# Kernel tuning notes

Hardware: AMD Instinct MI355X
Metric: run time of the kernel (lower is better)

Reference implementation:

```python
import jax, jax.numpy as jnp
import numpy as np

N_NODES = 50000

def _gat_layer(x, src, dst, W, a_l, a_r, bias, alpha, agg, act, n_nodes):
    # x: [N, in]; W: [in, H*F]; a_l, a_r: [H, F]; bias: [H*F]
    H, F = a_l.shape
    z = (x @ W).reshape(n_nodes, H, F)                      # [N,H,F]
    el = jnp.einsum('nhf,hf->nh', z, a_l)                   # [N,H]
    er = jnp.einsum('nhf,hf->nh', z, a_r)                   # [N,H]
    e = jax.nn.leaky_relu(el[src] + er[dst], alpha)         # [E,H]
    # segment softmax over in-edges of each destination node
    m = jax.ops.segment_max(e, dst, num_segments=n_nodes)   # [N,H]
    ex = jnp.exp(e - m[dst])                                # [E,H]
    s = jax.ops.segment_sum(ex, dst, num_segments=n_nodes)  # [N,H]
    attn = ex / jnp.maximum(s[dst], 1e-9)                   # [E,H]
    msg = attn[:, :, None] * z[src]                         # [E,H,F]
    h = jax.ops.segment_sum(msg, dst, num_segments=n_nodes) # [N,H,F]
    # identity residual (in_feats == H*F) as in DGL GATConv
    h = h + x.reshape(n_nodes, -1, F)
    h = h + bias.reshape(1, H, F)
    if agg == 'flatten':
        h = h.reshape(n_nodes, H * F)
    else:  # mean over heads
        h = h.mean(axis=1)
    if act is not None:
        h = act(h)
    return h


def setup_inputs() -> dict:
    key = jax.random.key(0)
    ks = jax.random.split(key, 14)
    N, E, D = N_NODES, 800000, 128
    H, F = 4, 32
    sc_in = 1.0 / np.sqrt(D)
    sc_h = 1.0 / np.sqrt(H * F)
    inp = {
        'feats': jax.random.normal(ks[0], (N, D), jnp.float32),
        'src': jax.random.randint(ks[1], (E,), 0, N),
        'dst': jax.random.randint(ks[2], (E,), 0, N),
        'W1': jax.random.normal(ks[3], (D, H * F), jnp.float32) * sc_in,
        'al1': jax.random.normal(ks[4], (H, F), jnp.float32) * sc_h,
        'ar1': jax.random.normal(ks[5], (H, F), jnp.float32) * sc_h,
        'b1': jnp.zeros((H * F,), jnp.float32),
        'W2': jax.random.normal(ks[6], (H * F, H * F), jnp.float32) * sc_h,
        'al2': jax.random.normal(ks[7], (H, F), jnp.float32) * sc_h,
        'ar2': jax.random.normal(ks[8], (H, F), jnp.float32) * sc_h,
        'b2': jnp.zeros((H * F,), jnp.float32),
        'Wp': jax.random.normal(ks[9], (F, 1), jnp.float32) / np.sqrt(F),
        'bp': jnp.zeros((1,), jnp.float32),
    }
    return inp


def reference(feats, src, dst, W1, al1, ar1, b1, W2, al2, ar2, b2, Wp, bp):
    h = _gat_layer(feats, src, dst, W1, al1, ar1, b1, 0.2, 'flatten', jax.nn.elu, N_NODES)
    h = _gat_layer(h, src, dst, W2, al2, ar2, b2, 0.2, 'mean', None, N_NODES)
    return h @ Wp + bp  # [N, 1]
```

## Files before the change

### kernel.cpp

```cpp
#include <hip/hip_runtime.h>
#include <hip/hip_bf16.h>

#define NN 50000
#define NE 800000
#define HF 128
#define MAXDEG 64

#define OFF_FLAG   0u
#define OFF_Z      16668672u
#define OFF_H1     29468672u
#define OFF_EL     42268672u
#define OFF_ER     43068672u
#define OFF_FILL   54000128u
#define OFF_ADJ2   60000000u

typedef __hip_bfloat16 bf16;
typedef unsigned short us16;

#define SCAT_B 3125
#define GEMM_B 782

typedef __attribute__((ext_vector_type(8))) short bf16x8;
typedef __attribute__((ext_vector_type(4))) float f32x4;

__device__ __forceinline__ float us2f(us16 u) {
  union { unsigned int i; float f; } c; c.i = ((unsigned int)u) << 16; return c.f;
}
__device__ __forceinline__ us16 f2us(float f) {
  bf16 h = __float2bfloat16(f);
  union { bf16 h; us16 u; } c; c.h = h; return c.u;
}
__device__ __forceinline__ float blo(unsigned v) {
  union { unsigned i; float f; } c; c.i = v << 16; return c.f;
}
__device__ __forceinline__ float bhi(unsigned v) {
  union { unsigned i; float f; } c; c.i = v & 0xffff0000u; return c.f;
}
__device__ __forceinline__ unsigned pk2(float a, float b) {
  return (unsigned)f2us(a) | ((unsigned)f2us(b) << 16);
}

__device__ __forceinline__ int detect_f32(const us16* __restrict__ u) {
  int t = threadIdx.x;
  int mx = 0;
  for (int i = t; i < 2048; i += 256) {
    int e = (u[i] >> 7) & 0xFF;
    mx = mx > e ? mx : e;
  }
#pragma unroll
  for (int m = 32; m >= 1; m >>= 1) {
    int o = __shfl_xor(mx, m);
    mx = mx > o ? mx : o;
  }
  __shared__ int sred[4];
  if ((t & 63) == 0) sred[t >> 6] = mx;
  __syncthreads();
  int a = sred[0] > sred[1] ? sred[0] : sred[1];
  int b = sred[2] > sred[3] ? sred[2] : sred[3];
  int r = a > b ? a : b;
  return r >= 135;
}

template <int LAYER>
__global__ __launch_bounds__(256) void k_gemm(
    const void* __restrict__ Xv, const void* __restrict__ Wv,
    const void* __restrict__ alr, const void* __restrict__ arr,
    us16* __restrict__ Z, float* __restrict__ el, float* __restrict__ er,
    const int* __restrict__ src, const int* __restrict__ dst,
    int* __restrict__ fill, int* __restrict__ adj2, int* __restrict__ flagp) {
  if (LAYER == 1) {
    if ((int)blockIdx.x < SCAT_B) {
      int e = blockIdx.x * 256 + threadIdx.x;
      int d = dst[e];
      int r = atomicAdd(&fill[d], 1);
      if (r < MAXDEG) adj2[(d << 6) + r] = src[e];
      return;
    }
  }
  int bx = (LAYER == 1) ? (int)blockIdx.x - SCAT_B : (int)blockIdx.x;

  __shared__ us16 Wl[HF * HF];
  int f;
  if (LAYER == 1) {
    f = detect_f32((const us16*)Wv);
    if (bx == 0 && threadIdx.x == 0) *flagp = f;
  } else {
    f = *flagp;
  }

  int tid = threadIdx.x;
  {
    const float* Wf = (const float*)Wv;
    const us16* Wb = (const us16*)Wv;
    for (int e = tid; e < HF * HF; e += 256) {
      int k = e >> 7, n = e & 127;
      int d = ((((k >> 5) * 8 + (n >> 4)) * 4 + ((k >> 3) & 3)) * 16 + (n & 15)) * 8 + (k & 7);
      Wl[d] = f ? f2us(Wf[e]) : Wb[e];
    }
  }
  __syncthreads();

  int w = tid >> 6;
  int lane = tid & 63;
  int q = lane >> 4;
  int c = lane & 15;
  int m0 = bx * 64 + w * 16;

  int rA = m0 + c;
  if (rA >= NN) rA = NN - 1;
  const us16* xb = (const us16*)Xv + (size_t)rA * HF;
  const float* xf = (const float*)Xv + (size_t)rA * HF;

  f32x4 acc[8] = {};
#pragma unroll
  for (int s = 0; s < 4; ++s) {
    bf16x8 a;
    if (LAYER == 1 && f) {
      float4 v0 = *(const float4*)&xf[s * 32 + q * 8];
      float4 v1 = *(const float4*)&xf[s * 32 + q * 8 + 4];
      union { us16 u[8]; bf16x8 v; } cv;
      cv.u[0] = f2us(v0.x); cv.u[1] = f2us(v0.y);
      cv.u[2] = f2us(v0.z); cv.u[3] = f2us(v0.w);
      cv.u[4] = f2us(v1.x); cv.u[5] = f2us(v1.y);
      cv.u[6] = f2us(v1.z); cv.u[7] = f2us(v1.w);
      a = cv.v;
    } else {
      a = *(const bf16x8*)&xb[s * 32 + q * 8];
    }
#pragma unroll
    for (int t = 0; t < 8; ++t) {
      bf16x8 bb = *(const bf16x8*)&Wl[((((s * 8) + t) * 4 + q) * 16 + c) * 8];
      acc[t] = __builtin_amdgcn_mfma_f32_16x16x32_bf16(a, bb, acc[t], 0, 0, 0);
    }
  }

#pragma unroll
  for (int reg = 0; reg < 4; ++reg) {
    int row = m0 + q * 4 + reg;
    if (row < NN) {
      us16* zrow = Z + (size_t)row * HF;
#pragma unroll
      for (int t = 0; t < 8; ++t) zrow[t * 16 + c] = f2us(acc[t][reg]);
    }
  }

  float alv[8], arv[8];
  {
    const float* alf = (const float*)alr; const us16* alb = (const us16*)alr;
    const float* arf = (const float*)arr; const us16* arb = (const us16*)arr;
#pragma unroll
    for (int t = 0; t < 8; ++t) {
      alv[t] = f ? alf[t * 16 + c] : us2f(alb[t * 16 + c]);
      arv[t] = f ? arf[t * 16 + c] : us2f(arb[t * 16 + c]);
    }
  }
#pragma unroll
  for (int reg = 0; reg < 4; ++reg) {
    int row = m0 + q * 4 + reg;
    float pl[4], pr[4];
#pragma unroll
    for (int h = 0; h < 4; ++h) {
      pl[h] = acc[2 * h][reg] * alv[2 * h] + acc[2 * h + 1][reg] * alv[2 * h + 1];
      pr[h] = acc[2 * h][reg] * arv[2 * h] + acc[2 * h + 1][reg] * arv[2 * h + 1];
    }
#pragma unroll
    for (int m = 1; m < 16; m <<= 1) {
#pragma unroll
      for (int h = 0; h < 4; ++h) {
        pl[h] += __shfl_xor(pl[h], m);
        pr[h] += __shfl_xor(pr[h], m);
      }
    }
    if (row < NN) {
      int cc = c & 3;
      float vl = cc == 0 ? pl[0] : cc == 1 ? pl[1] : cc == 2 ? pl[2] : pl[3];
      float vr = cc == 0 ? pr[0] : cc == 1 ? pr[1] : cc == 2 ? pr[2] : pr[3];
      if (c < 4) el[row * 4 + cc] = vl;
      else if (c < 8) er[row * 4 + cc] = vr;
    }
  }
}

template <int LAYER>
__global__ __launch_bounds__(256) void k_agg(
    const us16* __restrict__ Z, const float* __restrict__ el,
    const float* __restrict__ er, const int* __restrict__ fill,
    const int* __restrict__ adj2, const void* __restrict__ resid,
    const void* __restrict__ bias, us16* __restrict__ Hout,
    const void* __restrict__ Wp, const void* __restrict__ bp,
    void* __restrict__ out, const int* __restrict__ flag) {
  int f = *flag;
  int n = blockIdx.x * 4 + (threadIdx.x >> 6);
  int lane = threadIdx.x & 63;
  int g = lane >> 4;
  int p = lane & 15;
  int hl = p >> 2;
  int f0 = p * 8;
  int deg = fill[n];
  if (deg > MAXDEG) deg = MAXDEG;
  int begin = n << 6;
  float erh = er[n * 4 + hl];

  float acc[8] = {};
  float ssum = 0.f;
  int i = g;
  for (; i + 4 < deg; i += 8) {
    int s0 = adj2[begin + i];
    int s1 = adj2[begin + i + 4];
    float l0 = el[s0 * 4 + hl];
    float l1 = el[s1 * 4 + hl];
    uint4 za = *(const uint4*)&Z[(size_t)s0 * HF + f0];
    uint4 zb = *(const uint4*)&Z[(size_t)s1 * HF + f0];
    float sc0 = l0 + erh; sc0 = sc0 > 0.f ? sc0 : 0.2f * sc0;
    float sc1 = l1 + erh; sc1 = sc1 > 0.f ? sc1 : 0.2f * sc1;
    float ex0 = __expf(sc0);
    float ex1 = __expf(sc1);
    ssum += ex0 + ex1;
    acc[0] = fmaf(ex0, blo(za.x), acc[0]); acc[1] = fmaf(ex0, bhi(za.x), acc[1]);
    acc[2] = fmaf(ex0, blo(za.y), acc[2]); acc[3] = fmaf(ex0, bhi(za.y), acc[3]);
    acc[4] = fmaf(ex0, blo(za.z), acc[4]); acc[5] = fmaf(ex0, bhi(za.z), acc[5]);
    acc[6] = fmaf(ex0, blo(za.w), acc[6]); acc[7] = fmaf(ex0, bhi(za.w), acc[7]);
    acc[0] = fmaf(ex1, blo(zb.x), acc[0]); acc[1] = fmaf(ex1, bhi(zb.x), acc[1]);
    acc[2] = fmaf(ex1, blo(zb.y), acc[2]); acc[3] = fmaf(ex1, bhi(zb.y), acc[3]);
    acc[4] = fmaf(ex1, blo(zb.z), acc[4]); acc[5] = fmaf(ex1, bhi(zb.z), acc[5]);
    acc[6] = fmaf(ex1, blo(zb.w), acc[6]); acc[7] = fmaf(ex1, bhi(zb.w), acc[7]);
  }
  if (i < deg) {
    int s = adj2[begin + i];
    float sc = el[s * 4 + hl] + erh;
    sc = sc > 0.f ? sc : 0.2f * sc;
    float ex = __expf(sc);
    ssum += ex;
    uint4 zq = *(const uint4*)&Z[(size_t)s * HF + f0];
    acc[0] = fmaf(ex, blo(zq.x), acc[0]); acc[1] = fmaf(ex, bhi(zq.x), acc[1]);
    acc[2] = fmaf(ex, blo(zq.y), acc[2]); acc[3] = fmaf(ex, bhi(zq.y), acc[3]);
    acc[4] = fmaf(ex, blo(zq.z), acc[4]); acc[5] = fmaf(ex, bhi(zq.z), acc[5]);
    acc[6] = fmaf(ex, blo(zq.w), acc[6]); acc[7] = fmaf(ex, bhi(zq.w), acc[7]);
  }
  ssum += __shfl_xor(ssum, 16); ssum += __shfl_xor(ssum, 32);
#pragma unroll
  for (int j = 0; j < 8; ++j) {
    acc[j] += __shfl_xor(acc[j], 16);
    acc[j] += __shfl_xor(acc[j], 32);
  }
  float inv = 1.f / fmaxf(ssum, 1e-9f);

  float rx[8];
  if (LAYER == 1 && f) {
    const float* rf = (const float*)resid + (size_t)n * HF + f0;
    float4 r0 = *(const float4*)rf;
    float4 r1 = *(const float4*)(rf + 4);
    rx[0] = r0.x; rx[1] = r0.y; rx[2] = r0.z; rx[3] = r0.w;
    rx[4] = r1.x; rx[5] = r1.y; rx[6] = r1.z; rx[7] = r1.w;
  } else {
    uint4 xq = *(const uint4*)((const us16*)resid + (size_t)n * HF + f0);
    rx[0] = blo(xq.x); rx[1] = bhi(xq.x); rx[2] = blo(xq.y); rx[3] = bhi(xq.y);
    rx[4] = blo(xq.z); rx[5] = bhi(xq.z); rx[6] = blo(xq.w); rx[7] = bhi(xq.w);
  }
  float bv[8];
  if (f) {
    const float* bf_ = (const float*)bias + f0;
    bv[0] = bf_[0]; bv[1] = bf_[1]; bv[2] = bf_[2]; bv[3] = bf_[3];
    bv[4] = bf_[4]; bv[5] = bf_[5]; bv[6] = bf_[6]; bv[7] = bf_[7];
  } else {
    uint4 bq = *(const uint4*)((const us16*)bias + f0);
    bv[0] = blo(bq.x); bv[1] = bhi(bq.x); bv[2] = blo(bq.y); bv[3] = bhi(bq.y);
    bv[4] = blo(bq.z); bv[5] = bhi(bq.z); bv[6] = blo(bq.w); bv[7] = bhi(bq.w);
  }
  float t0 = fmaf(acc[0], inv, rx[0] + bv[0]);
  float t1 = fmaf(acc[1], inv, rx[1] + bv[1]);
  float t2 = fmaf(acc[2], inv, rx[2] + bv[2]);
  float t3 = fmaf(acc[3], inv, rx[3] + bv[3]);
  float t4 = fmaf(acc[4], inv, rx[4] + bv[4]);
  float t5 = fmaf(acc[5], inv, rx[5] + bv[5]);
  float t6 = fmaf(acc[6], inv, rx[6] + bv[6]);
  float t7 = fmaf(acc[7], inv, rx[7] + bv[7]);

  if (LAYER == 1) {
    t0 = t0 > 0.f ? t0 : __expf(t0) - 1.f;
    t1 = t1 > 0.f ? t1 : __expf(t1) - 1.f;
    t2 = t2 > 0.f ? t2 : __expf(t2) - 1.f;
    t3 = t3 > 0.f ? t3 : __expf(t3) - 1.f;
    t4 = t4 > 0.f ? t4 : __expf(t4) - 1.f;
    t5 = t5 > 0.f ? t5 : __expf(t5) - 1.f;
    t6 = t6 > 0.f ? t6 : __expf(t6) - 1.f;
    t7 = t7 > 0.f ? t7 : __expf(t7) - 1.f;
    if (g == 0) {
      uint4 o;
      o.x = pk2(t0, t1); o.y = pk2(t2, t3); o.z = pk2(t4, t5); o.w = pk2(t6, t7);
      *(uint4*)&Hout[(size_t)n * HF + f0] = o;
    }
  } else {
    t0 += __shfl_xor(t0, 4); t0 += __shfl_xor(t0, 8);
    t1 += __shfl_xor(t1, 4); t1 += __shfl_xor(t1, 8);
    t2 += __shfl_xor(t2, 4); t2 += __shfl_xor(t2, 8);
    t3 += __shfl_xor(t3, 4); t3 += __shfl_xor(t3, 8);
    t4 += __shfl_xor(t4, 4); t4 += __shfl_xor(t4, 8);
    t5 += __shfl_xor(t5, 4); t5 += __shfl_xor(t5, 8);
    t6 += __shfl_xor(t6, 4); t6 += __shfl_xor(t6, 8);
    t7 += __shfl_xor(t7, 4); t7 += __shfl_xor(t7, 8);
    int fw = (p & 3) * 8;
    float wv0, wv1, wv2, wv3, wv4, wv5, wv6, wv7;
    if (f) {
      const float* wpf = (const float*)Wp;
      wv0 = wpf[fw];     wv1 = wpf[fw + 1]; wv2 = wpf[fw + 2]; wv3 = wpf[fw + 3];
      wv4 = wpf[fw + 4]; wv5 = wpf[fw + 5]; wv6 = wpf[fw + 6]; wv7 = wpf[fw + 7];
    } else {
      const us16* wpb = (const us16*)Wp;
      wv0 = us2f(wpb[fw]);     wv1 = us2f(wpb[fw + 1]);
      wv2 = us2f(wpb[fw + 2]); wv3 = us2f(wpb[fw + 3]);
      wv4 = us2f(wpb[fw + 4]); wv5 = us2f(wpb[fw + 5]);
      wv6 = us2f(wpb[fw + 6]); wv7 = us2f(wpb[fw + 7]);
    }
    float pr = 0.25f * (t0 * wv0 + t1 * wv1 + t2 * wv2 + t3 * wv3 +
                        t4 * wv4 + t5 * wv5 + t6 * wv6 + t7 * wv7);
    pr += __shfl_xor(pr, 1); pr += __shfl_xor(pr, 2);
    if (lane == 0) {
      float bpv = f ? ((const float*)bp)[0] : us2f(((const us16*)bp)[0]);
      float res = pr + bpv;
      if (f) ((float*)out)[n] = res;
      else ((us16*)out)[n] = f2us(res);
    }
  }
}

extern "C" void kernel_launch(void* const* d_in, const int* in_sizes, int n_in,
                              void* d_out, int out_size, void* d_ws, size_t ws_size,
                              hipStream_t stream) {
  const int* src = (const int*)d_in[1];
  const int* dst = (const int*)d_in[2];
  char* ws = (char*)d_ws;
  int* flag   = (int*)(ws + OFF_FLAG);
  us16* z     = (us16*)(ws + OFF_Z);
  us16* h1    = (us16*)(ws + OFF_H1);
  float* el   = (float*)(ws + OFF_EL);
  float* er   = (float*)(ws + OFF_ER);
  int* fill   = (int*)(ws + OFF_FILL);
  int* adj2   = (int*)(ws + OFF_ADJ2);

  hipMemsetAsync(fill, 0, (size_t)NN * 4, stream);

  hipLaunchKernelGGL((k_gemm<1>), dim3(SCAT_B + GEMM_B), dim3(256), 0, stream,
                     d_in[0], d_in[3], d_in[4], d_in[5], z, el, er,
                     src, dst, fill, adj2, flag);
  hipLaunchKernelGGL((k_agg<1>), dim3(NN / 4), dim3(256), 0, stream, z, el, er,
                     fill, adj2, d_in[0], d_in[6], h1,
                     (const void*)nullptr, (const void*)nullptr, (void*)nullptr, flag);
  hipLaunchKernelGGL((k_gemm<2>), dim3(GEMM_B), dim3(256), 0, stream,
                     h1, d_in[7], d_in[8], d_in[9], z, el, er,
                     src, dst, fill, adj2, flag);
  hipLaunchKernelGGL((k_agg<2>), dim3(NN / 4), dim3(256), 0, stream, z, el, er,
                     fill, adj2, h1, d_in[10], (us16*)nullptr,
                     d_in[11], d_in[12], d_out, flag);
}
```

Before: 283.0 us.

## Fuse edge scatter into GEMM blocks and store adjacency as 16-bit indices

Instead of separate scatter blocks, each layer-1 GEMM block now loads four edges per thread with vector loads, issues the degree atomics before the MFMA loop, and writes the bucketed source ids after the epilogue, overlapping atomic latency with compute. The adjacency list is stored as 16-bit node ids, halving its write and read traffic in the aggregation kernels. This relies on node count fitting in 16 bits and on the edge count being a multiple of four.

```diff
diff --git a/kernel.cpp b/kernel.cpp
--- a/kernel.cpp
+++ b/kernel.cpp
@@ -17,7 +17,6 @@
 typedef __hip_bfloat16 bf16;
 typedef unsigned short us16;
 
-#define SCAT_B 3125
 #define GEMM_B 782
 
 typedef __attribute__((ext_vector_type(8))) short bf16x8;
@@ -67,28 +66,30 @@
     const void* __restrict__ alr, const void* __restrict__ arr,
     us16* __restrict__ Z, float* __restrict__ el, float* __restrict__ er,
     const int* __restrict__ src, const int* __restrict__ dst,
-    int* __restrict__ fill, int* __restrict__ adj2, int* __restrict__ flagp) {
+    int* __restrict__ fill, us16* __restrict__ adj2, int* __restrict__ flagp) {
+  int tid = threadIdx.x;
+  int bx = (int)blockIdx.x;
+
+  int4 dstv = {0, 0, 0, 0}, srcv = {0, 0, 0, 0};
+  bool ed = false;
   if (LAYER == 1) {
-    if ((int)blockIdx.x < SCAT_B) {
-      int e = blockIdx.x * 256 + threadIdx.x;
-      int d = dst[e];
-      int r = atomicAdd(&fill[d], 1);
-      if (r < MAXDEG) adj2[(d << 6) + r] = src[e];
-      return;
-    }
-  }
-  int bx = (LAYER == 1) ? (int)blockIdx.x - SCAT_B : (int)blockIdx.x;
+    int e0 = (bx * 256 + tid) * 4;
+    if (e0 < NE) {
+      ed = true;
+      dstv = *(const int4*)&dst[e0];
+      srcv = *(const int4*)&src[e0];
+    }
+  }
 
   __shared__ us16 Wl[HF * HF];
   int f;
   if (LAYER == 1) {
     f = detect_f32((const us16*)Wv);
-    if (bx == 0 && threadIdx.x == 0) *flagp = f;
+    if (bx == 0 && tid == 0) *flagp = f;
   } else {
     f = *flagp;
   }
 
-  int tid = threadIdx.x;
   {
     const float* Wf = (const float*)Wv;
     const us16* Wb = (const us16*)Wv;
@@ -111,10 +112,9 @@
   const us16* xb = (const us16*)Xv + (size_t)rA * HF;
   const float* xf = (const float*)Xv + (size_t)rA * HF;
 
-  f32x4 acc[8] = {};
+  bf16x8 afr[4];
 #pragma unroll
   for (int s = 0; s < 4; ++s) {
-    bf16x8 a;
     if (LAYER == 1 && f) {
       float4 v0 = *(const float4*)&xf[s * 32 + q * 8];
       float4 v1 = *(const float4*)&xf[s * 32 + q * 8 + 4];
@@ -123,14 +123,38 @@
       cv.u[2] = f2us(v0.z); cv.u[3] = f2us(v0.w);
       cv.u[4] = f2us(v1.x); cv.u[5] = f2us(v1.y);
       cv.u[6] = f2us(v1.z); cv.u[7] = f2us(v1.w);
-      a = cv.v;
+      afr[s] = cv.v;
     } else {
-      a = *(const bf16x8*)&xb[s * 32 + q * 8];
-    }
+      afr[s] = *(const bf16x8*)&xb[s * 32 + q * 8];
+    }
+  }
+  float alv[8], arv[8];
+  {
+    const float* alf = (const float*)alr; const us16* alb = (const us16*)alr;
+    const float* arf = (const float*)arr; const us16* arb = (const us16*)arr;
+#pragma unroll
+    for (int t = 0; t < 8; ++t) {
+      alv[t] = f ? alf[t * 16 + c] : us2f(alb[t * 16 + c]);
+      arv[t] = f ? arf[t * 16 + c] : us2f(arb[t * 16 + c]);
+    }
+  }
+
+  int r0 = 0, r1 = 0, r2 = 0, r3 = 0;
+  if (LAYER == 1 && ed) {
+    r0 = atomicAdd(&fill[dstv.x], 1);
+    r1 = atomicAdd(&fill[dstv.y], 1);
+    r2 = atomicAdd(&fill[dstv.z], 1);
+    r3 = atomicAdd(&fill[dstv.w], 1);
+  }
+  asm volatile("" ::: "memory");
+
+  f32x4 acc[8] = {};
+#pragma unroll
+  for (int s = 0; s < 4; ++s) {
 #pragma unroll
     for (int t = 0; t < 8; ++t) {
       bf16x8 bb = *(const bf16x8*)&Wl[((((s * 8) + t) * 4 + q) * 16 + c) * 8];
-      acc[t] = __builtin_amdgcn_mfma_f32_16x16x32_bf16(a, bb, acc[t], 0, 0, 0);
+      acc[t] = __builtin_amdgcn_mfma_f32_16x16x32_bf16(afr[s], bb, acc[t], 0, 0, 0);
     }
   }
 
@@ -144,16 +168,6 @@
     }
   }
 
-  float alv[8], arv[8];
-  {
-    const float* alf = (const float*)alr; const us16* alb = (const us16*)alr;
-    const float* arf = (const float*)arr; const us16* arb = (const us16*)arr;
-#pragma unroll
-    for (int t = 0; t < 8; ++t) {
-      alv[t] = f ? alf[t * 16 + c] : us2f(alb[t * 16 + c]);
-      arv[t] = f ? arf[t * 16 + c] : us2f(arb[t * 16 + c]);
-    }
-  }
 #pragma unroll
   for (int reg = 0; reg < 4; ++reg) {
     int row = m0 + q * 4 + reg;
@@ -179,13 +193,20 @@
       else if (c < 8) er[row * 4 + cc] = vr;
     }
   }
+
+  if (LAYER == 1 && ed) {
+    if (r0 < MAXDEG) adj2[(dstv.x << 6) + r0] = (us16)srcv.x;
+    if (r1 < MAXDEG) adj2[(dstv.y << 6) + r1] = (us16)srcv.y;
+    if (r2 < MAXDEG) adj2[(dstv.z << 6) + r2] = (us16)srcv.z;
+    if (r3 < MAXDEG) adj2[(dstv.w << 6) + r3] = (us16)srcv.w;
+  }
 }
 
 template <int LAYER>
 __global__ __launch_bounds__(256) void k_agg(
     const us16* __restrict__ Z, const float* __restrict__ el,
     const float* __restrict__ er, const int* __restrict__ fill,
-    const int* __restrict__ adj2, const void* __restrict__ resid,
+    const us16* __restrict__ adj2, const void* __restrict__ resid,
     const void* __restrict__ bias, us16* __restrict__ Hout,
     const void* __restrict__ Wp, const void* __restrict__ bp,
     void* __restrict__ out, const int* __restrict__ flag) {
@@ -336,11 +357,11 @@
   float* el   = (float*)(ws + OFF_EL);
   float* er   = (float*)(ws + OFF_ER);
   int* fill   = (int*)(ws + OFF_FILL);
-  int* adj2   = (int*)(ws + OFF_ADJ2);
+  us16* adj2  = (us16*)(ws + OFF_ADJ2);
 
   hipMemsetAsync(fill, 0, (size_t)NN * 4, stream);
 
-  hipLaunchKernelGGL((k_gemm<1>), dim3(SCAT_B + GEMM_B), dim3(256), 0, stream,
+  hipLaunchKernelGGL((k_gemm<1>), dim3(GEMM_B), dim3(256), 0, stream,
                      d_in[0], d_in[3], d_in[4], d_in[5], z, el, er,
                      src, dst, fill, adj2, flag);
   hipLaunchKernelGGL((k_agg<1>), dim3(NN / 4), dim3(256), 0, stream, z, el, er,
```

After: 269.0 us. 5.0% less time.

## Store adjacency as 16-bit indices and broadcast neighbor lists via shuffles

Applied to the files above, without the earlier changes.

Narrows the padded adjacency list from int32 to uint16, halving its storage and read traffic. The aggregation kernel now loads the whole 64-entry neighbor row with one coalesced load per wave and hands indices to lanes with shuffles. The tail branch is replaced by predicated iterations. The scatter is split out of the layer-1 GEMM kernel into its own launch, which adds a launch and removes overlap between the two. Truncating to 16 bits is incorrect for node indices of 65536 or more; N=50000 fits, so this is safe only for this node count.

```diff
diff --git a/kernel.cpp b/kernel.cpp
--- a/kernel.cpp
+++ b/kernel.cpp
@@ -61,34 +61,33 @@
   return r >= 135;
 }
 
+__global__ __launch_bounds__(256) void k_scatter(
+    const int* __restrict__ src, const int* __restrict__ dst,
+    int* __restrict__ fill, us16* __restrict__ adj2) {
+  int e = blockIdx.x * 256 + threadIdx.x;
+  int d = dst[e];
+  int r = atomicAdd(&fill[d], 1);
+  if (r < MAXDEG) adj2[(d << 6) + r] = (us16)src[e];
+}
+
 template <int LAYER>
 __global__ __launch_bounds__(256) void k_gemm(
     const void* __restrict__ Xv, const void* __restrict__ Wv,
     const void* __restrict__ alr, const void* __restrict__ arr,
     us16* __restrict__ Z, float* __restrict__ el, float* __restrict__ er,
-    const int* __restrict__ src, const int* __restrict__ dst,
-    int* __restrict__ fill, int* __restrict__ adj2, int* __restrict__ flagp) {
-  if (LAYER == 1) {
-    if ((int)blockIdx.x < SCAT_B) {
-      int e = blockIdx.x * 256 + threadIdx.x;
-      int d = dst[e];
-      int r = atomicAdd(&fill[d], 1);
-      if (r < MAXDEG) adj2[(d << 6) + r] = src[e];
-      return;
-    }
-  }
-  int bx = (LAYER == 1) ? (int)blockIdx.x - SCAT_B : (int)blockIdx.x;
+    int* __restrict__ flagp) {
+  int tid = threadIdx.x;
+  int bx = (int)blockIdx.x;
 
   __shared__ us16 Wl[HF * HF];
   int f;
   if (LAYER == 1) {
     f = detect_f32((const us16*)Wv);
-    if (bx == 0 && threadIdx.x == 0) *flagp = f;
+    if (bx == 0 && tid == 0) *flagp = f;
   } else {
     f = *flagp;
   }
 
-  int tid = threadIdx.x;
   {
     const float* Wf = (const float*)Wv;
     const us16* Wb = (const us16*)Wv;
@@ -185,7 +184,7 @@
 __global__ __launch_bounds__(256) void k_agg(
     const us16* __restrict__ Z, const float* __restrict__ el,
     const float* __restrict__ er, const int* __restrict__ fill,
-    const int* __restrict__ adj2, const void* __restrict__ resid,
+    const us16* __restrict__ adj2, const void* __restrict__ resid,
     const void* __restrict__ bias, us16* __restrict__ Hout,
     const void* __restrict__ Wp, const void* __restrict__ bp,
     void* __restrict__ out, const int* __restrict__ flag) {
@@ -196,25 +195,33 @@
   int p = lane & 15;
   int hl = p >> 2;
   int f0 = p * 8;
+  int begin = n << 6;
+
+  int sl = (int)adj2[begin + lane];
+
   int deg = fill[n];
   if (deg > MAXDEG) deg = MAXDEG;
-  int begin = n << 6;
   float erh = er[n * 4 + hl];
 
   float acc[8] = {};
   float ssum = 0.f;
-  int i = g;
-  for (; i + 4 < deg; i += 8) {
-    int s0 = adj2[begin + i];
-    int s1 = adj2[begin + i + 4];
+  for (int k = 0; k * 8 < deg; ++k) {
+    int i0 = g + k * 8;
+    int i1 = i0 + 4;
+    int s0 = __shfl(sl, i0);
+    int s1 = __shfl(sl, i1);
+    bool v0 = i0 < deg;
+    bool v1 = i1 < deg;
+    s0 = v0 ? s0 : 0;
+    s1 = v1 ? s1 : 0;
     float l0 = el[s0 * 4 + hl];
     float l1 = el[s1 * 4 + hl];
     uint4 za = *(const uint4*)&Z[(size_t)s0 * HF + f0];
     uint4 zb = *(const uint4*)&Z[(size_t)s1 * HF + f0];
     float sc0 = l0 + erh; sc0 = sc0 > 0.f ? sc0 : 0.2f * sc0;
     float sc1 = l1 + erh; sc1 = sc1 > 0.f ? sc1 : 0.2f * sc1;
-    float ex0 = __expf(sc0);
-    float ex1 = __expf(sc1);
+    float ex0 = v0 ? __expf(sc0) : 0.f;
+    float ex1 = v1 ? __expf(sc1) : 0.f;
     ssum += ex0 + ex1;
     acc[0] = fmaf(ex0, blo(za.x), acc[0]); acc[1] = fmaf(ex0, bhi(za.x), acc[1]);
     acc[2] = fmaf(ex0, blo(za.y), acc[2]); acc[3] = fmaf(ex0, bhi(za.y), acc[3]);
@@ -224,18 +231,6 @@
     acc[2] = fmaf(ex1, blo(zb.y), acc[2]); acc[3] = fmaf(ex1, bhi(zb.y), acc[3]);
     acc[4] = fmaf(ex1, blo(zb.z), acc[4]); acc[5] = fmaf(ex1, bhi(zb.z), acc[5]);
     acc[6] = fmaf(ex1, blo(zb.w), acc[6]); acc[7] = fmaf(ex1, bhi(zb.w), acc[7]);
-  }
-  if (i < deg) {
-    int s = adj2[begin + i];
-    float sc = el[s * 4 + hl] + erh;
-    sc = sc > 0.f ? sc : 0.2f * sc;
-    float ex = __expf(sc);
-    ssum += ex;
-    uint4 zq = *(const uint4*)&Z[(size_t)s * HF + f0];
-    acc[0] = fmaf(ex, blo(zq.x), acc[0]); acc[1] = fmaf(ex, bhi(zq.x), acc[1]);
-    acc[2] = fmaf(ex, blo(zq.y), acc[2]); acc[3] = fmaf(ex, bhi(zq.y), acc[3]);
-    acc[4] = fmaf(ex, blo(zq.z), acc[4]); acc[5] = fmaf(ex, bhi(zq.z), acc[5]);
-    acc[6] = fmaf(ex, blo(zq.w), acc[6]); acc[7] = fmaf(ex, bhi(zq.w), acc[7]);
   }
   ssum += __shfl_xor(ssum, 16); ssum += __shfl_xor(ssum, 32);
 #pragma unroll
@@ -336,19 +331,19 @@
   float* el   = (float*)(ws + OFF_EL);
   float* er   = (float*)(ws + OFF_ER);
   int* fill   = (int*)(ws + OFF_FILL);
-  int* adj2   = (int*)(ws + OFF_ADJ2);
+  us16* adj2  = (us16*)(ws + OFF_ADJ2);
 
   hipMemsetAsync(fill, 0, (size_t)NN * 4, stream);
 
-  hipLaunchKernelGGL((k_gemm<1>), dim3(SCAT_B + GEMM_B), dim3(256), 0, stream,
-                     d_in[0], d_in[3], d_in[4], d_in[5], z, el, er,
-                     src, dst, fill, adj2, flag);
+  hipLaunchKernelGGL(k_scatter, dim3(SCAT_B), dim3(256), 0, stream,
+                     src, dst, fill, adj2);
+  hipLaunchKernelGGL((k_gemm<1>), dim3(GEMM_B), dim3(256), 0, stream,
+                     d_in[0], d_in[3], d_in[4], d_in[5], z, el, er, flag);
   hipLaunchKernelGGL((k_agg<1>), dim3(NN / 4), dim3(256), 0, stream, z, el, er,
                      fill, adj2, d_in[0], d_in[6], h1,
                      (const void*)nullptr, (const void*)nullptr, (void*)nullptr, flag);
   hipLaunchKernelGGL((k_gemm<2>), dim3(GEMM_B), dim3(256), 0, stream,
-                     h1, d_in[7], d_in[8], d_in[9], z, el, er,
-                     src, dst, fill, adj2, flag);
+                     h1, d_in[7], d_in[8], d_in[9], z, el, er, flag);
   hipLaunchKernelGGL((k_agg<2>), dim3(NN / 4), dim3(256), 0, stream, z, el, er,
                      fill, adj2, h1, d_in[10], (us16*)nullptr,
                      d_in[11], d_in[12], d_out, flag);
```

Result: faster. 268.3 us (-5.2%).
